# Performance work log

Measured on AMD Instinct MI355X. Metric: run time of the kernel, lower is better.

## Reference

```python
import jax, jax.numpy as jnp
import numpy as np

ENC_H = 512      # encoder_hidden_dim -> encoder_out feature = 2*ENC_H
DEC_H = 512      # decoder_hidden_dim
B, S = 32, 2048  # batch, max_seq_len


def setup_inputs() -> dict:
    key = jax.random.key(0)
    k1, k2, k3, k4, k5, k6, k7 = jax.random.split(key, 7)
    encoder_out = jax.random.normal(k1, (B, S, 2 * ENC_H), dtype=jnp.float32)
    hidden = jax.random.normal(k2, (B, DEC_H), dtype=jnp.float32)
    lengths = jax.random.randint(k3, (B,), 1, S + 1, dtype=jnp.int64)
    in_dim = 2 * ENC_H + DEC_H
    # torch nn.Linear default init scale
    attn_w = jax.random.uniform(k4, (DEC_H, in_dim), jnp.float32, -1.0, 1.0) / np.sqrt(in_dim)
    attn_b = jax.random.uniform(k5, (DEC_H,), jnp.float32, -1.0, 1.0) / np.sqrt(in_dim)
    v_w = jax.random.uniform(k6, (1, DEC_H), jnp.float32, -1.0, 1.0) / np.sqrt(DEC_H)
    v_b = jax.random.uniform(k7, (1,), jnp.float32, -1.0, 1.0) / np.sqrt(DEC_H)
    return {"encoder_out": encoder_out, "hidden": hidden, "lengths": lengths,
            "attn_w": attn_w, "attn_b": attn_b, "v_w": v_w, "v_b": v_b}


def reference(encoder_out, hidden, lengths, attn_w, attn_b, v_w, v_b):
    # encoder_out: [B,S,2E], hidden: [B,D], lengths: [B]
    Bc, Sc, _ = encoder_out.shape
    h = jnp.broadcast_to(hidden[:, None, :], (Bc, Sc, hidden.shape[-1]))
    temp = jnp.concatenate([h, encoder_out], axis=2)           # [B,S,D+2E]
    e = jnp.tanh(jnp.einsum('bsf,df->bsd', temp, attn_w) + attn_b)  # [B,S,D]
    scores = jnp.einsum('bsd,d->bs', e, v_w[0]) + v_b[0]       # [B,S]
    mask = jnp.arange(Sc)[None, :] < lengths[:, None]          # [B,S]
    scores = jnp.where(mask, scores, -jnp.inf)
    energy = jax.nn.softmax(scores, axis=1)                    # softmax over valid positions
    energy = jnp.where(mask, energy, 0.0)                      # padded positions stay exactly 0
    context = jnp.einsum('bs,bse->be', energy, encoder_out)    # [B,2E]
    return context
```

## Files before the change

kernel.cpp:

```cpp
#include <hip/hip_runtime.h>
#include <hip/hip_bf16.h>
#include <math.h>

typedef __attribute__((ext_vector_type(8))) short short8;
typedef __attribute__((ext_vector_type(16))) float f32x16;

static constexpr int B  = 32;
static constexpr int S  = 2048;
static constexpr int D  = 512;
static constexpr int KE = 1024;
static constexpr int IN = 1536;

__device__ __forceinline__ unsigned pk2(float lo, float hi) {
    __hip_bfloat162 t = __float22bfloat162_rn(make_float2(lo, hi));
    unsigned u;
    __builtin_memcpy(&u, &t, 4);
    return u;
}

__device__ __forceinline__ short8 pack8(float4 f0, float4 f1) {
    unsigned u[4] = { pk2(f0.x, f0.y), pk2(f0.z, f0.w), pk2(f1.x, f1.y), pk2(f1.z, f1.w) };
    short8 r;
    __builtin_memcpy(&r, u, 16);
    return r;
}

__device__ __forceinline__ float tanh_fast(float x) {
    float e = __expf(2.0f * x);
    return (e - 1.0f) * __builtin_amdgcn_rcpf(e + 1.0f);
}

typedef const __attribute__((address_space(1))) unsigned int guint;
typedef __attribute__((address_space(3))) unsigned int luint;
__device__ __forceinline__ void gload_lds16(const void* g, void* l) {
    __builtin_amdgcn_global_load_lds((guint*)g, (luint*)l, 16, 0, 0);
}

__global__ void k_prep(const float* __restrict__ attn_w,
                       const float* __restrict__ hidden,
                       const float* __restrict__ attn_b,
                       unsigned short* __restrict__ Bf,
                       float* __restrict__ u,
                       float* __restrict__ num,
                       float* __restrict__ den) {
    if (blockIdx.x < 256) {
        int o = blockIdx.x * 256 + threadIdx.x;
        int l6  = o & 63;
        int grp = o >> 6;
        int d = (grp & 15) * 32 + (l6 & 31);
        int k = (grp >> 4) * 16 + (l6 >> 5) * 8;
        const float* src = attn_w + (size_t)d * IN + 512 + k;
        float4 f0 = *(const float4*)src;
        float4 f1 = *(const float4*)(src + 4);
        ((short8*)Bf)[o] = pack8(f0, f1);
    } else {
        int bx = blockIdx.x - 256;
        {
            int gid = bx * 256 + threadIdx.x;
            ((float2*)num)[gid] = make_float2(0.f, 0.f);
            if (bx == 0 && threadIdx.x < 32) den[threadIdx.x] = 0.f;
        }
        int b  = bx >> 1;
        int dh = bx & 1;
        int w  = threadIdx.x >> 6;
        int l  = threadIdx.x & 63;
        int j  = l & 15;
        int dsub = l >> 4;
        const float* h = hidden + b * D;
        float4 hv[8];
        #pragma unroll
        for (int i = 0; i < 8; i++) hv[i] = *(const float4*)(h + i * 64 + j * 4);
        #pragma unroll
        for (int p = 0; p < 16; p++) {
            int d = dh * 256 + p * 16 + w * 4 + dsub;
            const float* wr = attn_w + (size_t)d * IN + j * 4;
            float a = 0.f;
            #pragma unroll
            for (int i = 0; i < 8; i++) {
                float4 wv = *(const float4*)(wr + i * 64);
                a += hv[i].x * wv.x + hv[i].y * wv.y + hv[i].z * wv.z + hv[i].w * wv.w;
            }
            #pragma unroll
            for (int off = 8; off >= 1; off >>= 1) a += __shfl_xor(a, off);
            if (j == 0) u[b * D + d] = a + attn_b[d];
        }
    }
}

#define LOADB(K, DST) do {                                     \
    _Pragma("unroll")                                          \
    for (int _jt = 0; _jt < 4; _jt++)                          \
        DST[_jt] = bb[(size_t)(K) * 1024 + _jt * 64];          \
} while (0)

__global__ __launch_bounds__(256, 2) void k_fused(
    const float* __restrict__ enc, const unsigned short* __restrict__ Bfrag,
    const float* __restrict__ u, const float* __restrict__ v_w,
    const float* __restrict__ v_b, const int* __restrict__ lengths,
    float* __restrict__ num, float* __restrict__ den)
{
    __shared__ float4 ldsA[2][2048];
    float* sPart = (float*)&ldsA[0][0];
    float* sExp  = sPart + 256;

    const int b   = blockIdx.y;
    const int s0  = blockIdx.x * 64;
    const int len = lengths[b];
    if (s0 >= len) return;

    const int tid = threadIdx.x;
    const int w   = tid >> 6;
    const int l   = tid & 63;

    const float* encb = enc + ((size_t)b * S + s0) * KE;

    const int rlo  = l >> 5;
    const int xv   = (l & 31) ^ (2 * w + rlo);
    const float* aSrc = encb + (size_t)(2 * w + rlo) * KE + 4 * xv;

    const short8* bb = (const short8*)Bfrag + (w * 4) * 64 + l;

    f32x16 acc[2][4];
    #pragma unroll
    for (int mt = 0; mt < 2; mt++)
        #pragma unroll
        for (int jt = 0; jt < 4; jt++)
            #pragma unroll
            for (int e = 0; e < 16; e++) acc[mt][jt][e] = 0.f;

    short8 pb[2][4];
    LOADB(0, pb[0]);
    LOADB(1, pb[1]);

    const int m0  = l & 31;
    const int xr  = m0 & 7;
    const int hi2 = (l >> 5) * 2;

    #pragma unroll
    for (int i = 0; i < 8; i++)
        gload_lds16(aSrc + (size_t)i * 8 * KE, (void*)&ldsA[0][(i * 4 + w) * 64]);

    #pragma unroll 1
    for (int c = 0; c < 8; ++c) {
        __syncthreads();
        if (c < 7) {
            const float* src = aSrc + (c + 1) * 128;
            float4* bufn = ldsA[(c + 1) & 1];
            #pragma unroll
            for (int i = 0; i < 8; i++)
                gload_lds16(src + (size_t)i * 8 * KE, (void*)&bufn[(i * 4 + w) * 64]);
        }
        const float4* bf = &ldsA[c & 1][0];
        #pragma unroll
        for (int t = 0; t < 8; ++t) {
            const int s0l = t * 4 + hi2;
            const int p0  = s0l ^ xr;
            const int p1  = (s0l + 1) ^ xr;
            float4 f00 = bf[m0 * 32 + p0];
            float4 f01 = bf[m0 * 32 + p1];
            float4 f10 = bf[(m0 + 32) * 32 + p0];
            float4 f11 = bf[(m0 + 32) * 32 + p1];
            short8 a0 = pack8(f00, f01);
            short8 a1 = pack8(f10, f11);
            const int bp = t & 1;
            #pragma unroll
            for (int jt = 0; jt < 4; jt++) {
                acc[0][jt] = __builtin_amdgcn_mfma_f32_32x32x16_bf16(a0, pb[bp][jt], acc[0][jt], 0, 0, 0);
                acc[1][jt] = __builtin_amdgcn_mfma_f32_32x32x16_bf16(a1, pb[bp][jt], acc[1][jt], 0, 0, 0);
            }
            LOADB((c * 8 + t + 2) & 63, pb[bp]);
        }
    }

    float vv[4], uu[4];
    const float* ub = u + b * D;
    #pragma unroll
    for (int jt = 0; jt < 4; jt++) {
        int d = w * 128 + jt * 32 + (l & 31);
        vv[jt] = v_w[d];
        uu[jt] = ub[d];
    }
    float red[2][16];
    #pragma unroll
    for (int mt = 0; mt < 2; mt++)
        #pragma unroll
        for (int r = 0; r < 16; r++) {
            float s = 0.f;
            #pragma unroll
            for (int jt = 0; jt < 4; jt++)
                s += vv[jt] * tanh_fast(acc[mt][jt][r] + uu[jt]);
            red[mt][r] = s;
        }
    #pragma unroll
    for (int off = 16; off >= 1; off >>= 1)
        #pragma unroll
        for (int mt = 0; mt < 2; mt++)
            #pragma unroll
            for (int r = 0; r < 16; r++)
                red[mt][r] += __shfl_xor(red[mt][r], off);
    if ((l & 31) == 0) {
        int hb = (l >> 5) * 4;
        #pragma unroll
        for (int mt = 0; mt < 2; mt++)
            #pragma unroll
            for (int r = 0; r < 16; r++)
                sPart[w * 64 + mt * 32 + (r & 3) + 8 * (r >> 2) + hb] = red[mt][r];
    }
    __syncthreads();

    if (tid < 64) {
        float sc = sPart[tid] + sPart[64 + tid] + sPart[128 + tid] + sPart[192 + tid] + v_b[0];
        float wexp = (s0 + tid < len) ? __expf(sc) : 0.f;
        sExp[tid] = wexp;
        #pragma unroll
        for (int off = 32; off >= 1; off >>= 1) wexp += __shfl_xor(wexp, off);
        if (tid == 0) atomicAdd(den + b, wexp);
    }
    __syncthreads();

    const float4* e4 = (const float4*)encb;
    float4 cacc[4];
    #pragma unroll
    for (int j = 0; j < 4; j++) cacc[j] = make_float4(0.f, 0.f, 0.f, 0.f);
    #pragma unroll
    for (int i = 0; i < 16; i++) {
        #pragma unroll
        for (int j = 0; j < 4; j++) {
            float wgt = sExp[i * 4 + j];
            float4 v = e4[(size_t)(i * 4 + j) * 256 + tid];
            cacc[j].x += wgt * v.x; cacc[j].y += wgt * v.y;
            cacc[j].z += wgt * v.z; cacc[j].w += wgt * v.w;
        }
    }
    #pragma unroll
    for (int j = 1; j < 4; j++) {
        cacc[0].x += cacc[j].x; cacc[0].y += cacc[j].y;
        cacc[0].z += cacc[j].z; cacc[0].w += cacc[j].w;
    }
    float* o = num + b * KE + tid * 4;
    atomicAdd(o + 0, cacc[0].x);
    atomicAdd(o + 1, cacc[0].y);
    atomicAdd(o + 2, cacc[0].z);
    atomicAdd(o + 3, cacc[0].w);
}

__global__ void k_norm(const float* __restrict__ num, const float* __restrict__ den,
                       float* __restrict__ out) {
    int b = blockIdx.x;
    int t = threadIdx.x;
    float inv = 1.f / den[b];
    float4 v = ((const float4*)(num + b * KE))[t];
    v.x *= inv; v.y *= inv; v.z *= inv; v.w *= inv;
    ((float4*)(out + b * KE))[t] = v;
}

extern "C" void kernel_launch(void* const* d_in, const int* in_sizes, int n_in,
                              void* d_out, int out_size, void* d_ws, size_t ws_size,
                              hipStream_t stream) {
    const float* enc    = (const float*)d_in[0];
    const float* hidden = (const float*)d_in[1];
    const int*   lengths= (const int*)d_in[2];
    const float* attn_w = (const float*)d_in[3];
    const float* attn_b = (const float*)d_in[4];
    const float* v_w    = (const float*)d_in[5];
    const float* v_b    = (const float*)d_in[6];
    float* out = (float*)d_out;

    float* ws  = (float*)d_ws;
    float* u   = ws;
    float* num = u + B * D;
    float* den = num + B * KE;
    unsigned short* Bf = (unsigned short*)(den + 32);

    k_prep <<<dim3(320), 256, 0, stream>>>(attn_w, hidden, attn_b, Bf, u, num, den);
    k_fused<<<dim3(S / 64, B), 256, 0, stream>>>(enc, Bf, u, v_w, v_b, lengths, num, den);
    k_norm <<<dim3(B), 256, 0, stream>>>(num, den, out);
}
```

Measured before the change: 439.0 us.

## Stage whole encoder tile as bf16 in LDS instead of double-buffered fp32 chunks

The fused kernel now loads the full 64x1024 encoder tile with ordinary global loads, converts it to bf16 once, and stores it into a swizzled 128 KB LDS tile. This replaces the double-buffered fp32 global-to-LDS streaming and removes the per-iteration conversion and barriers from the MFMA loop. The larger LDS footprint lowers occupancy to one block per CU, and the loads no longer overlap with compute. The prep kernel also splits the hidden projection across more blocks.

```diff
diff --git a/kernel.cpp b/kernel.cpp
--- a/kernel.cpp
+++ b/kernel.cpp
@@ -28,12 +28,6 @@
 __device__ __forceinline__ float tanh_fast(float x) {
     float e = __expf(2.0f * x);
     return (e - 1.0f) * __builtin_amdgcn_rcpf(e + 1.0f);
-}
-
-typedef const __attribute__((address_space(1))) unsigned int guint;
-typedef __attribute__((address_space(3))) unsigned int luint;
-__device__ __forceinline__ void gload_lds16(const void* g, void* l) {
-    __builtin_amdgcn_global_load_lds((guint*)g, (luint*)l, 16, 0, 0);
 }
 
 __global__ void k_prep(const float* __restrict__ attn_w,
@@ -55,13 +49,13 @@
         ((short8*)Bf)[o] = pack8(f0, f1);
     } else {
         int bx = blockIdx.x - 256;
-        {
+        if (bx < 64) {
             int gid = bx * 256 + threadIdx.x;
             ((float2*)num)[gid] = make_float2(0.f, 0.f);
             if (bx == 0 && threadIdx.x < 32) den[threadIdx.x] = 0.f;
         }
-        int b  = bx >> 1;
-        int dh = bx & 1;
+        int b  = bx >> 3;
+        int dh = bx & 7;
         int w  = threadIdx.x >> 6;
         int l  = threadIdx.x & 63;
         int j  = l & 15;
@@ -71,8 +65,8 @@
         #pragma unroll
         for (int i = 0; i < 8; i++) hv[i] = *(const float4*)(h + i * 64 + j * 4);
         #pragma unroll
-        for (int p = 0; p < 16; p++) {
-            int d = dh * 256 + p * 16 + w * 4 + dsub;
+        for (int p = 0; p < 4; p++) {
+            int d = dh * 64 + p * 16 + w * 4 + dsub;
             const float* wr = attn_w + (size_t)d * IN + j * 4;
             float a = 0.f;
             #pragma unroll
@@ -93,15 +87,15 @@
         DST[_jt] = bb[(size_t)(K) * 1024 + _jt * 64];          \
 } while (0)
 
-__global__ __launch_bounds__(256, 2) void k_fused(
+__global__ __launch_bounds__(256, 1) void k_fused(
     const float* __restrict__ enc, const unsigned short* __restrict__ Bfrag,
     const float* __restrict__ u, const float* __restrict__ v_w,
     const float* __restrict__ v_b, const int* __restrict__ lengths,
     float* __restrict__ num, float* __restrict__ den)
 {
-    __shared__ float4 ldsA[2][2048];
-    float* sPart = (float*)&ldsA[0][0];
-    float* sExp  = sPart + 256;
+    __shared__ short8 tile[64 * 128];
+    __shared__ float sPart[4][64];
+    __shared__ float sExp[64];
 
     const int b   = blockIdx.y;
     const int s0  = blockIdx.x * 64;
@@ -113,63 +107,53 @@
     const int l   = tid & 63;
 
     const float* encb = enc + ((size_t)b * S + s0) * KE;
-
-    const int rlo  = l >> 5;
-    const int xv   = (l & 31) ^ (2 * w + rlo);
-    const float* aSrc = encb + (size_t)(2 * w + rlo) * KE + 4 * xv;
-
     const short8* bb = (const short8*)Bfrag + (w * 4) * 64 + l;
-
-    f32x16 acc[2][4];
-    #pragma unroll
-    for (int mt = 0; mt < 2; mt++)
-        #pragma unroll
-        for (int jt = 0; jt < 4; jt++)
-            #pragma unroll
-            for (int e = 0; e < 16; e++) acc[mt][jt][e] = 0.f;
 
     short8 pb[2][4];
     LOADB(0, pb[0]);
     LOADB(1, pb[1]);
 
-    const int m0  = l & 31;
-    const int xr  = m0 & 7;
-    const int hi2 = (l >> 5) * 2;
-
-    #pragma unroll
-    for (int i = 0; i < 8; i++)
-        gload_lds16(aSrc + (size_t)i * 8 * KE, (void*)&ldsA[0][(i * 4 + w) * 64]);
-
-    #pragma unroll 1
-    for (int c = 0; c < 8; ++c) {
-        __syncthreads();
-        if (c < 7) {
-            const float* src = aSrc + (c + 1) * 128;
-            float4* bufn = ldsA[(c + 1) & 1];
-            #pragma unroll
-            for (int i = 0; i < 8; i++)
-                gload_lds16(src + (size_t)i * 8 * KE, (void*)&bufn[(i * 4 + w) * 64]);
-        }
-        const float4* bf = &ldsA[c & 1][0];
-        #pragma unroll
-        for (int t = 0; t < 8; ++t) {
-            const int s0l = t * 4 + hi2;
-            const int p0  = s0l ^ xr;
-            const int p1  = (s0l + 1) ^ xr;
-            float4 f00 = bf[m0 * 32 + p0];
-            float4 f01 = bf[m0 * 32 + p1];
-            float4 f10 = bf[(m0 + 32) * 32 + p0];
-            float4 f11 = bf[(m0 + 32) * 32 + p1];
-            short8 a0 = pack8(f00, f01);
-            short8 a1 = pack8(f10, f11);
-            const int bp = t & 1;
-            #pragma unroll
-            for (int jt = 0; jt < 4; jt++) {
-                acc[0][jt] = __builtin_amdgcn_mfma_f32_32x32x16_bf16(a0, pb[bp][jt], acc[0][jt], 0, 0, 0);
-                acc[1][jt] = __builtin_amdgcn_mfma_f32_32x32x16_bf16(a1, pb[bp][jt], acc[1][jt], 0, 0, 0);
-            }
-            LOADB((c * 8 + t + 2) & 63, pb[bp]);
-        }
+    {
+        const float* src0 = encb + (size_t)(16 * w) * KE + l * 8;
+        #pragma unroll 4
+        for (int i = 0; i < 32; ++i) {
+            int r = 16 * w + (i >> 1);
+            const float* s = src0 + (size_t)(i >> 1) * KE + (i & 1) * 512;
+            float4 f0 = *(const float4*)s;
+            float4 f1 = *(const float4*)(s + 4);
+            int un = (i & 1) * 64 + l;
+            tile[r * 128 + (un ^ (r & 7))] = pack8(f0, f1);
+        }
+    }
+
+    f32x16 acc[2][4];
+    #pragma unroll
+    for (int mt = 0; mt < 2; mt++)
+        #pragma unroll
+        for (int jt = 0; jt < 4; jt++)
+            #pragma unroll
+            for (int e = 0; e < 16; e++) acc[mt][jt][e] = 0.f;
+
+    const int m0 = l & 31;
+    const int xr = m0 & 7;
+    const int hi = l >> 5;
+    const short8* rowA = tile + m0 * 128;
+    const short8* rowB = tile + (m0 + 32) * 128;
+
+    __syncthreads();
+
+    #pragma unroll 4
+    for (int t = 0; t < 64; ++t) {
+        const int p = (t * 2 + hi) ^ xr;
+        short8 a0 = rowA[p];
+        short8 a1 = rowB[p];
+        const int bp = t & 1;
+        #pragma unroll
+        for (int jt = 0; jt < 4; jt++) {
+            acc[0][jt] = __builtin_amdgcn_mfma_f32_32x32x16_bf16(a0, pb[bp][jt], acc[0][jt], 0, 0, 0);
+            acc[1][jt] = __builtin_amdgcn_mfma_f32_32x32x16_bf16(a1, pb[bp][jt], acc[1][jt], 0, 0, 0);
+        }
+        LOADB((t + 2) & 63, pb[bp]);
     }
 
     float vv[4], uu[4];
@@ -204,12 +188,12 @@
         for (int mt = 0; mt < 2; mt++)
             #pragma unroll
             for (int r = 0; r < 16; r++)
-                sPart[w * 64 + mt * 32 + (r & 3) + 8 * (r >> 2) + hb] = red[mt][r];
+                sPart[w][mt * 32 + (r & 3) + 8 * (r >> 2) + hb] = red[mt][r];
     }
     __syncthreads();
 
     if (tid < 64) {
-        float sc = sPart[tid] + sPart[64 + tid] + sPart[128 + tid] + sPart[192 + tid] + v_b[0];
+        float sc = sPart[0][tid] + sPart[1][tid] + sPart[2][tid] + sPart[3][tid] + v_b[0];
         float wexp = (s0 + tid < len) ? __expf(sc) : 0.f;
         sExp[tid] = wexp;
         #pragma unroll
@@ -272,7 +256,7 @@
     float* den = num + B * KE;
     unsigned short* Bf = (unsigned short*)(den + 32);
 
-    k_prep <<<dim3(320), 256, 0, stream>>>(attn_w, hidden, attn_b, Bf, u, num, den);
+    k_prep <<<dim3(512), 256, 0, stream>>>(attn_w, hidden, attn_b, Bf, u, num, den);
     k_fused<<<dim3(S / 64, B), 256, 0, stream>>>(enc, Bf, u, v_w, v_b, lengths, num, den);
     k_norm <<<dim3(B), 256, 0, stream>>>(num, den, out);
 }
```

Measured after the change: 476.3 us. 8.5% more time.
